# Kernel optimization log

Measured on AMD Instinct MI355X. Metric: run time of the kernel, lower is better.

## Reference

```python
import jax, jax.numpy as jnp
import numpy as np

N_NODES = 16384   # dim_size (number of aggregation groups)
DEG = 16          # neighbors per node
H = 128           # hidden_dim
E = N_NODES * DEG # total neighbor rows


def setup_inputs() -> dict:
    key = jax.random.key(0)
    k1, k2, k3 = jax.random.split(key, 3)
    x = jax.random.normal(k1, (E, H), dtype=jnp.float32)
    # sorted segment ids, DEG neighbors per node (ragged in general; uniform here)
    index = jnp.repeat(jnp.arange(N_NODES, dtype=jnp.int32), DEG)
    # torch LSTM params: gates stacked [i, f, g, o] -> [4H, H]
    W_ih = jax.random.normal(k2, (4 * H, H), dtype=jnp.float32) * 0.02  # xavier gain=0.02 scale
    W_hh = jax.random.normal(k3, (4 * H, H), dtype=jnp.float32) * (1.0 / np.sqrt(H))
    b_ih = jnp.zeros((4 * H,), jnp.float32)
    b_hh = jnp.zeros((4 * H,), jnp.float32)
    return {"x": x, "index": index, "W_ih": W_ih, "W_hh": W_hh,
            "b_ih": b_ih, "b_hh": b_hh, "dim_size": N_NODES}


def reference(x, index, W_ih, W_hh, b_ih, b_hh, dim_size):
    # Faithful to LSTMAggregator.forward: per-group gather of neighbor rows,
    # single-layer LSTM over each group's sequence, final hidden state h_n
    # written to out[group]; empty groups stay zero. (The original's randperm
    # shuffle is nondeterministic and omitted: neighbors kept in index order.)
    x = jnp.nan_to_num(x, nan=0.0)
    E_, Hd = x.shape

    # --- pack ragged groups into a padded [N, L, H] tensor ---
    order = jnp.argsort(index, stable=True)
    idx_s = index[order]
    counts = jax.ops.segment_sum(jnp.ones((E_,), jnp.int32), idx_s, num_segments=dim_size)
    starts = jnp.cumsum(counts) - counts           # exclusive prefix sum
    pos = jnp.arange(E_, dtype=jnp.int32) - starts[idx_s]  # position within group
    L = int(jnp.max(counts))                       # static at call time (concrete inputs)

    x_s = x[order]
    padded = jnp.zeros((dim_size, L, Hd), x.dtype).at[idx_s, pos].set(x_s)  # [N, L, H]
    valid = jnp.arange(L)[None, :] < counts[:, None]                        # [N, L]

    # --- batched masked LSTM scan over time ---
    bias = b_ih + b_hh
    h0 = jnp.zeros((dim_size, Hd), x.dtype)

    def step(carry, inp):
        h, c = carry
        xt, m = inp                                 # xt: [N, H], m: [N]
        gates = xt @ W_ih.T + h @ W_hh.T + bias     # [N, 4H], gate order i,f,g,o
        i, f, g, o = jnp.split(gates, 4, axis=-1)
        i = jax.nn.sigmoid(i); f = jax.nn.sigmoid(f)
        g = jnp.tanh(g);       o = jax.nn.sigmoid(o)
        c_new = f * c + i * g
        h_new = o * jnp.tanh(c_new)
        m = m[:, None]
        return (jnp.where(m, h_new, h), jnp.where(m, c_new, c)), None

    xs = (jnp.swapaxes(padded, 0, 1), valid.T)      # time-major [L, N, H], [L, N]
    (h_final, _), _ = jax.lax.scan(step, (h0, h0), xs)
    return jnp.nan_to_num(h_final, nan=0.0)        # [dim_size, H]
```

## Files before the change

### kernel.cpp

```cpp
#include <hip/hip_runtime.h>

#define DEG      16
#define HDIM     128
#define MB       32
#define NTHREADS 512

typedef __attribute__((ext_vector_type(8))) short  short8;
typedef __attribute__((ext_vector_type(4))) float  floatx4;
typedef __attribute__((ext_vector_type(4))) unsigned int uintx4;

#define MFMA(A,B,C) __builtin_amdgcn_mfma_f32_16x16x32_bf16(A,B,C,0,0,0)
#define L2E  1.4426950408889634f
#define L2E2 2.8853900817779268f

__device__ __forceinline__ unsigned short f2bf(float f) {
  union { float f; unsigned int u; } v; v.f = f;
  unsigned int u = v.u;
  u += 0x7fffu + ((u >> 16) & 1u);
  return (unsigned short)(u >> 16);
}

__device__ __forceinline__ unsigned int cvtpk(float lo, float hi) {
  unsigned int r;
  asm("v_cvt_pk_bf16_f32 %0, %1, %2" : "=v"(r) : "v"(lo), "v"(hi));
  return r;
}

#if __has_builtin(__builtin_amdgcn_exp2f)
#define FEXP2(x) __builtin_amdgcn_exp2f(x)
#else
__device__ __forceinline__ float FEXP2_fn(float x) {
  float r; asm("v_exp_f32 %0, %1" : "=v"(r) : "v"(x)); return r;
}
#define FEXP2(x) FEXP2_fn(x)
#endif

__device__ __forceinline__ float fsig2(float s) {
  return __builtin_amdgcn_rcpf(1.0f + FEXP2(-s));
}
__device__ __forceinline__ float ftanh2(float s) {
  return 1.0f - 2.0f * __builtin_amdgcn_rcpf(1.0f + FEXP2(s));
}

__global__ void convert_w_kernel(const float* __restrict__ Wih,
                                 const float* __restrict__ Whh,
                                 unsigned short* __restrict__ Wsw) {
  int i    = blockIdx.x * 256 + threadIdx.x;
  int lane = i & 63;
  int frag = i >> 6;
  int kt = frag >> 5;
  int wg = frag & 31;
  int w  = wg >> 2;
  int g  = wg & 3;
  int j  = g * 128 + w * 16 + (lane & 15);
  int k0 = kt * 32 + (lane >> 4) * 8;
  float sc = (g == 2) ? L2E2 : L2E;
  const float* src = (k0 < HDIM) ? (Wih + (size_t)j * HDIM + k0)
                                 : (Whh + (size_t)j * HDIM + (k0 - HDIM));
  short8 o;
  #pragma unroll
  for (int e = 0; e < 8; ++e) o[e] = (short)f2bf(src[e] * sc);
  *(short8*)(Wsw + (size_t)i * 8) = o;
}


#define HPART(HOFF)                                                            \
  {                                                                            \
    const unsigned short* Wp = Wsw;                                            \
    asm volatile("" : "+s"(Wp));                     \
    _Pragma("unroll")                                                          \
    for (int kh = 0; kh < 4; ++kh) {                                           \
      const unsigned short* Wk = Wp + ((size_t)((4 + kh) * 32 + w_id * 4) * 64 + lane) * 8; \
      short8 bfr[4];                                                           \
      _Pragma("unroll")                                                        \
      for (int g = 0; g < 4; ++g) bfr[g] = *(const short8*)(Wk + g * 512);     \
      const char* hb = (kh & 1) ? hsO : hsE;                                   \
      short8 ah0 = *(const short8*)(hb + (HOFF) + 0    + kh * 64);             \
      short8 ah1 = *(const short8*)(hb + (HOFF) + 4096 + kh * 64);             \
      _Pragma("unroll")                                                        \
      for (int g = 0; g < 4; ++g) {                                            \
        acc[g][0] = MFMA(ah0, bfr[g], acc[g][0]);                              \
        acc[g][1] = MFMA(ah1, bfr[g], acc[g][1]);                              \
      }                                                                        \
    }                                                                          \
  }

#define ACT1(MT, WOFF, LAST_, CS)                                              \
  {                                                                            \
    float hv[4];                                                               \
    _Pragma("unroll")                                                          \
    for (int r = 0; r < 4; ++r) {                                              \
      float iv = fsig2 (acc[0][MT][r]);                                        \
      float fv = fsig2 (acc[1][MT][r]);                                        \
      float gv = ftanh2(acc[2][MT][r]);                                        \
      float ov = fsig2 (acc[3][MT][r]);                                        \
      float cn = fv * CS[r] + iv * gv;                                         \
      CS[r] = cn;                                                              \
      hv[r] = ov * ftanh2(L2E2 * cn);                                          \
    }                                                                          \
    if (LAST_) {                                                               \
      float* ob = out + (size_t)(node0 + (MT) * 16 + q * 4) * HDIM + j_g;      \
      _Pragma("unroll")                                                        \
      for (int r = 0; r < 4; ++r) ob[r * HDIM] = hv[r];                        \
    } else {                                                                   \
      unsigned int p01 = cvtpk(hv[0], hv[1]);                                  \
      unsigned int p23 = cvtpk(hv[2], hv[3]);                                  \
      *(unsigned short*)(hwp[0] + (WOFF) + (MT) * 4096) = (unsigned short)p01;         \
      *(unsigned short*)(hwp[1] + (WOFF) + (MT) * 4096) = (unsigned short)(p01 >> 16); \
      *(unsigned short*)(hwp[2] + (WOFF) + (MT) * 4096) = (unsigned short)p23;         \
      *(unsigned short*)(hwp[3] + (WOFF) + (MT) * 4096) = (unsigned short)(p23 >> 16); \
    }                                                                          \
  }

#define XPART(XOFF)                                                            \
  {                                                                            \
    const unsigned short* Wp = Wsw;                                            \
    asm volatile("" : "+s"(Wp));                                               \
    const unsigned short* Wx = Wp + ((size_t)(w_id * 256 + lane)) * 8;         \
    short8 wv[4]; short8 a0, a1;                                               \
                                    \
    _Pragma("unroll")                                                          \
    for (int g = 0; g < 4; ++g) wv[g] = *(const short8*)(Wx + g * 512);        \
    a0 = *(const short8*)(xsE + (XOFF) + 0);                                   \
    a1 = *(const short8*)(xsE + (XOFF) + 4096 + 0);                            \
    _Pragma("unroll")                                                          \
    for (int g = 0; g < 4; ++g) {                                              \
      acc[g][0] = MFMA(a0, wv[g], bias4[g]);                                   \
      acc[g][1] = MFMA(a1, wv[g], bias4[g]);                                   \
    }                                                                          \
                                                                 \
    _Pragma("unroll")                                                          \
    for (int g = 0; g < 4; ++g) wv[g] = *(const short8*)(Wx + 16384 + g * 512);\
    a0 = *(const short8*)(xsO + (XOFF) + 64);                                  \
    a1 = *(const short8*)(xsO + (XOFF) + 4096 + 64);                           \
    _Pragma("unroll")                                                          \
    for (int g = 0; g < 4; ++g) {                                              \
      acc[g][0] = MFMA(a0, wv[g], acc[g][0]);                                  \
      acc[g][1] = MFMA(a1, wv[g], acc[g][1]);                                  \
    }                                                                          \
                                                                \
    _Pragma("unroll")                                                          \
    for (int g = 0; g < 4; ++g) wv[g] = *(const short8*)(wlB + g * 1024);      \
    a0 = *(const short8*)(xsE + (XOFF) + 128);                                 \
    a1 = *(const short8*)(xsE + (XOFF) + 4096 + 128);                          \
    _Pragma("unroll")                                                          \
    for (int g = 0; g < 4; ++g) {                                              \
      acc[g][0] = MFMA(a0, wv[g], acc[g][0]);                                  \
      acc[g][1] = MFMA(a1, wv[g], acc[g][1]);                                  \
    }                                                                          \
                                                                 \
    _Pragma("unroll")                                                          \
    for (int g = 0; g < 4; ++g) wv[g] = *(const short8*)(Wx + 49152 + g * 512);\
    a0 = *(const short8*)(xsO + (XOFF) + 192);                                 \
    a1 = *(const short8*)(xsO + (XOFF) + 4096 + 192);                          \
    _Pragma("unroll")                                                          \
    for (int g = 0; g < 4; ++g) {                                              \
      acc[g][0] = MFMA(a0, wv[g], acc[g][0]);                                  \
      acc[g][1] = MFMA(a1, wv[g], acc[g][1]);                                  \
    }                                                                          \
  }

#define STEP(T, PAR, WITH_H, LAST_)                                            \
  {                                                                            \
    if (WITH_H) HPART((PAR) * 8192);                                           \
    ACT1(0, ((PAR) ^ 1) * 8192, LAST_, cs0)                                    \
    ACT1(1, ((PAR) ^ 1) * 8192, LAST_, cs1)                                    \
    if (!(LAST_)) {                                                            \
      XPART((((PAR) ^ 1)) * 8192)                                              \
      if ((T) + 2 < DEG) {                                                     \
        uintx4 p;                                                              \
        p[0] = cvtpk(xp0[0], xp0[1]); p[1] = cvtpk(xp0[2], xp0[3]);            \
        p[2] = cvtpk(xp1[0], xp1[1]); p[3] = cvtpk(xp1[2], xp1[3]);            \
        *(uintx4*)(xsW + (PAR) * 8192) = p;                                    \
        if ((T) + 3 < DEG) {                                                   \
          const float* xq_ = xb0 + (size_t)((T) + 3) * HDIM;                   \
          xp0 = ((const floatx4*)xq_)[0]; xp1 = ((const floatx4*)xq_)[1];      \
        }                                                                      \
      }                                                                        \
    }                                                                          \
    __syncthreads();                                                           \
  }

__global__ __launch_bounds__(NTHREADS, 4)
void lstm_agg_kernel(const float* __restrict__ x,
                     const float* __restrict__ b_ih,
                     const float* __restrict__ b_hh,
                     const unsigned short* __restrict__ Wsw,
                     float* __restrict__ out) {
  __shared__ __align__(16) unsigned short Xs[2 * MB * HDIM];
  __shared__ __align__(16) unsigned short Hs[2 * MB * HDIM];
  __shared__ __align__(16) unsigned short Wl[32 * 512];

  const int tid  = threadIdx.x;
  const int w_id = tid >> 6;
  const int lane = tid & 63;
  const int l15  = lane & 15;
  const int q    = lane >> 4;
  const int node0 = blockIdx.x * MB;
  const int j_g = w_id * 16 + l15;

  floatx4 bias4[4];
  #pragma unroll
  for (int g = 0; g < 4; ++g) {
    float b = (b_ih[g * 128 + j_g] + b_hh[g * 128 + j_g]) * ((g == 2) ? L2E2 : L2E);
    floatx4 bv = {b, b, b, b};
    bias4[g] = bv;
  }

  #pragma unroll
  for (int i = 0; i < 4; ++i) {
    int o = tid * 32 + i * 8;
    *(short8*)&Wl[o] = *(const short8*)(Wsw + 2 * 32 * 512 + o);
  }

  const int fA  = (l15 & 7) ^ ((l15 & 8) >> 2);
  const int qx  = (q ^ (fA & 3)) << 4;
  const int f64 = (fA >> 2) << 6;
  const char* xsE = (const char*)Xs + l15 * 256 + qx + f64;
  const char* xsO = (const char*)Xs + l15 * 256 + qx - f64;
  const char* hsE = (const char*)Hs + l15 * 256 + qx + f64;
  const char* hsO = (const char*)Hs + l15 * 256 + qx - f64;

  const char* wlB = (const char*)Wl + w_id * 4096 + lane * 16;

  const int hc  = j_g >> 3;
  const int hkl = j_g & 7;
  char* hwp[4];
  #pragma unroll
  for (int r = 0; r < 4; ++r) {
    int m  = q * 4 + r;
    int fr = (m & 7) ^ ((m & 8) >> 2);
    hwp[r] = (char*)Hs + m * 256 + ((hc ^ fr) << 4) + hkl * 2;
  }

  const int m_x = tid >> 4;
  const int kc  = tid & 15;
  const int fX  = (m_x & 7) ^ ((m_x & 8) >> 2);
  const float* xb0 = x + ((size_t)(node0 + m_x) * DEG) * HDIM + kc * 8;
  char* xsW = (char*)Xs + m_x * 256 + ((kc ^ fX) << 4);

  floatx4 cs0 = {0.f, 0.f, 0.f, 0.f};
  floatx4 cs1 = {0.f, 0.f, 0.f, 0.f};
  floatx4 acc[4][2];
  floatx4 xp0, xp1;

  {
    floatx4 u0 = ((const floatx4*)xb0)[0], u1 = ((const floatx4*)xb0)[1];
    uintx4 p;
    p[0] = cvtpk(u0[0], u0[1]); p[1] = cvtpk(u0[2], u0[3]);
    p[2] = cvtpk(u1[0], u1[1]); p[3] = cvtpk(u1[2], u1[3]);
    *(uintx4*)xsW = p;
    u0 = ((const floatx4*)(xb0 + HDIM))[0]; u1 = ((const floatx4*)(xb0 + HDIM))[1];
    p[0] = cvtpk(u0[0], u0[1]); p[1] = cvtpk(u0[2], u0[3]);
    p[2] = cvtpk(u1[0], u1[1]); p[3] = cvtpk(u1[2], u1[3]);
    *(uintx4*)(xsW + 8192) = p;
    xp0 = ((const floatx4*)(xb0 + 2 * HDIM))[0];
    xp1 = ((const floatx4*)(xb0 + 2 * HDIM))[1];
  }
  __syncthreads();

  XPART(0)
  __syncthreads();

  STEP(0, 0, 0, 0)
  #pragma unroll 1
  for (int t = 1; t < 15; t += 2) {
    STEP(t,     1, 1, 0)
    STEP(t + 1, 0, 1, 0)
  }
  STEP(15, 1, 1, 1)
}

extern "C" void kernel_launch(void* const* d_in, const int* in_sizes, int n_in,
                              void* d_out, int out_size, void* d_ws, size_t ws_size,
                              hipStream_t stream) {
  const float* x   = (const float*)d_in[0];
  const float* Wih = (const float*)d_in[2];
  const float* Whh = (const float*)d_in[3];
  const float* bih = (const float*)d_in[4];
  const float* bhh = (const float*)d_in[5];
  unsigned short* Wsw = (unsigned short*)d_ws;
  float* out = (float*)d_out;

  hipLaunchKernelGGL(convert_w_kernel, dim3(64), dim3(256), 0, stream, Wih, Whh, Wsw);

  int nodes   = in_sizes[0] / (DEG * HDIM);
  int nblocks = nodes / MB;
  hipLaunchKernelGGL(lstm_agg_kernel, dim3(nblocks), dim3(NTHREADS), 0, stream,
                     x, bih, bhh, Wsw, out);
}
```

Baseline: 284.8 us.

## Process two 32-node tiles per block and interleave their gate activations with input MFMAs

Each block now handles 64 nodes as two 32-node sub-tiles. The recurrent MFMA pass covers both tiles, and one tile's activations are interleaved with the other tile's input-projection MFMAs so transcendental work overlaps matrix work. Three W_ih k-slices are held in registers, and a second W_hh slice moves into LDS using 128 KB of dynamic shared memory. The bias is added in the activation step instead of seeding the accumulator. In exchange, occupancy drops to 2 blocks per CU, register pressure rises, and the grid has half as many blocks.

Result: faster. 262.6 us (-7.8%).

```diff
diff --git a/kernel.cpp b/kernel.cpp
--- a/kernel.cpp
+++ b/kernel.cpp
@@ -2,7 +2,7 @@
 
 #define DEG      16
 #define HDIM     128
-#define MB       32
+#define MB       64
 #define NTHREADS 512
 
 typedef __attribute__((ext_vector_type(8))) short  short8;
@@ -26,14 +26,9 @@
   return r;
 }
 
-#if __has_builtin(__builtin_amdgcn_exp2f)
-#define FEXP2(x) __builtin_amdgcn_exp2f(x)
-#else
-__device__ __forceinline__ float FEXP2_fn(float x) {
+__device__ __forceinline__ float FEXP2(float x) {
   float r; asm("v_exp_f32 %0, %1" : "=v"(r) : "v"(x)); return r;
 }
-#define FEXP2(x) FEXP2_fn(x)
-#endif
 
 __device__ __forceinline__ float fsig2(float s) {
   return __builtin_amdgcn_rcpf(1.0f + FEXP2(-s));
@@ -64,132 +59,143 @@
 }
 
 
-#define HPART(HOFF)                                                            \
+#define HPART_BOTH(PAR)                                                        \
   {                                                                            \
     const unsigned short* Wp = Wsw;                                            \
     asm volatile("" : "+s"(Wp));                     \
     _Pragma("unroll")                                                          \
     for (int kh = 0; kh < 4; ++kh) {                                           \
-      const unsigned short* Wk = Wp + ((size_t)((4 + kh) * 32 + w_id * 4) * 64 + lane) * 8; \
       short8 bfr[4];                                                           \
-      _Pragma("unroll")                                                        \
-      for (int g = 0; g < 4; ++g) bfr[g] = *(const short8*)(Wk + g * 512);     \
+      if (kh == 2) {                                                           \
+        _Pragma("unroll")                                                      \
+        for (int g = 0; g < 4; ++g) bfr[g] = *(const short8*)(wlB6 + g * 1024);\
+      } else {                                                                 \
+        const unsigned short* Wk = Wp + ((size_t)((4 + kh) * 32 + w_id * 4) * 64 + lane) * 8; \
+        _Pragma("unroll")                                                      \
+        for (int g = 0; g < 4; ++g) bfr[g] = *(const short8*)(Wk + g * 512);   \
+      }                                                                        \
       const char* hb = (kh & 1) ? hsO : hsE;                                   \
-      short8 ah0 = *(const short8*)(hb + (HOFF) + 0    + kh * 64);             \
-      short8 ah1 = *(const short8*)(hb + (HOFF) + 4096 + kh * 64);             \
+      short8 a00 = *(const short8*)(hb + (PAR) * 16384 + 0     + kh * 64);     \
+      short8 a01 = *(const short8*)(hb + (PAR) * 16384 + 4096  + kh * 64);     \
+      short8 a10 = *(const short8*)(hb + (PAR) * 16384 + 8192  + kh * 64);     \
+      short8 a11 = *(const short8*)(hb + (PAR) * 16384 + 12288 + kh * 64);     \
       _Pragma("unroll")                                                        \
       for (int g = 0; g < 4; ++g) {                                            \
-        acc[g][0] = MFMA(ah0, bfr[g], acc[g][0]);                              \
-        acc[g][1] = MFMA(ah1, bfr[g], acc[g][1]);                              \
+        acc[0][g][0] = MFMA(a00, bfr[g], acc[0][g][0]);                        \
+        acc[0][g][1] = MFMA(a01, bfr[g], acc[0][g][1]);                        \
+        acc[1][g][0] = MFMA(a10, bfr[g], acc[1][g][0]);                        \
+        acc[1][g][1] = MFMA(a11, bfr[g], acc[1][g][1]);                        \
       }                                                                        \
     }                                                                          \
   }
 
-#define ACT1(MT, WOFF, LAST_, CS)                                              \
+#define ACT1(TAU, MT, WOFF, LAST_)                                             \
   {                                                                            \
     float hv[4];                                                               \
     _Pragma("unroll")                                                          \
     for (int r = 0; r < 4; ++r) {                                              \
-      float iv = fsig2 (acc[0][MT][r]);                                        \
-      float fv = fsig2 (acc[1][MT][r]);                                        \
-      float gv = ftanh2(acc[2][MT][r]);                                        \
-      float ov = fsig2 (acc[3][MT][r]);                                        \
-      float cn = fv * CS[r] + iv * gv;                                         \
-      CS[r] = cn;                                                              \
+      float iv = fsig2 (acc[TAU][0][MT][r] + bias[0]);                         \
+      float fv = fsig2 (acc[TAU][1][MT][r] + bias[1]);                         \
+      float gv = ftanh2(acc[TAU][2][MT][r] + bias[2]);                         \
+      float ov = fsig2 (acc[TAU][3][MT][r] + bias[3]);                         \
+      float cn = fv * cs[TAU][MT][r] + iv * gv;                                \
+      cs[TAU][MT][r] = cn;                                                     \
       hv[r] = ov * ftanh2(L2E2 * cn);                                          \
     }                                                                          \
     if (LAST_) {                                                               \
-      float* ob = out + (size_t)(node0 + (MT) * 16 + q * 4) * HDIM + j_g;      \
+      float* ob = outB + (TAU) * 4096 + (MT) * 2048;                           \
       _Pragma("unroll")                                                        \
       for (int r = 0; r < 4; ++r) ob[r * HDIM] = hv[r];                        \
     } else {                                                                   \
       unsigned int p01 = cvtpk(hv[0], hv[1]);                                  \
       unsigned int p23 = cvtpk(hv[2], hv[3]);                                  \
-      *(unsigned short*)(hwp[0] + (WOFF) + (MT) * 4096) = (unsigned short)p01;         \
-      *(unsigned short*)(hwp[1] + (WOFF) + (MT) * 4096) = (unsigned short)(p01 >> 16); \
-      *(unsigned short*)(hwp[2] + (WOFF) + (MT) * 4096) = (unsigned short)p23;         \
-      *(unsigned short*)(hwp[3] + (WOFF) + (MT) * 4096) = (unsigned short)(p23 >> 16); \
-    }                                                                          \
-  }
-
-#define XPART(XOFF)                                                            \
-  {                                                                            \
-    const unsigned short* Wp = Wsw;                                            \
-    asm volatile("" : "+s"(Wp));                                               \
-    const unsigned short* Wx = Wp + ((size_t)(w_id * 256 + lane)) * 8;         \
-    short8 wv[4]; short8 a0, a1;                                               \
-                                    \
-    _Pragma("unroll")                                                          \
-    for (int g = 0; g < 4; ++g) wv[g] = *(const short8*)(Wx + g * 512);        \
-    a0 = *(const short8*)(xsE + (XOFF) + 0);                                   \
-    a1 = *(const short8*)(xsE + (XOFF) + 4096 + 0);                            \
+      *(unsigned short*)(hwp[0] + (WOFF) + (TAU) * 8192 + (MT) * 4096) = (unsigned short)p01;         \
+      *(unsigned short*)(hwp[1] + (WOFF) + (TAU) * 8192 + (MT) * 4096) = (unsigned short)(p01 >> 16); \
+      *(unsigned short*)(hwp[2] + (WOFF) + (TAU) * 8192 + (MT) * 4096) = (unsigned short)p23;         \
+      *(unsigned short*)(hwp[3] + (WOFF) + (TAU) * 8192 + (MT) * 4096) = (unsigned short)(p23 >> 16); \
+    }                                                                          \
+  }
+
+#define XPART1(TAU, XOFF)                                                      \
+  {                                                                            \
+    floatx4 z4 = {0.0f, 0.0f, 0.0f, 0.0f};                                     \
+    short8 a0, a1, wv[4];                                                      \
+                                                   \
+    a0 = *(const short8*)(xsE + (XOFF) + (TAU) * 8192 + 0);                    \
+    a1 = *(const short8*)(xsE + (XOFF) + (TAU) * 8192 + 4096 + 0);             \
     _Pragma("unroll")                                                          \
     for (int g = 0; g < 4; ++g) {                                              \
-      acc[g][0] = MFMA(a0, wv[g], bias4[g]);                                   \
-      acc[g][1] = MFMA(a1, wv[g], bias4[g]);                                   \
-    }                                                                          \
-                                                                 \
-    _Pragma("unroll")                                                          \
-    for (int g = 0; g < 4; ++g) wv[g] = *(const short8*)(Wx + 16384 + g * 512);\
-    a0 = *(const short8*)(xsO + (XOFF) + 64);                                  \
-    a1 = *(const short8*)(xsO + (XOFF) + 4096 + 64);                           \
+      acc[TAU][g][0] = MFMA(a0, breg[0][g], z4);                               \
+      acc[TAU][g][1] = MFMA(a1, breg[0][g], z4);                               \
+    }                                                                          \
+                                                               \
+    a0 = *(const short8*)(xsO + (XOFF) + (TAU) * 8192 + 64);                   \
+    a1 = *(const short8*)(xsO + (XOFF) + (TAU) * 8192 + 4096 + 64);            \
     _Pragma("unroll")                                                          \
     for (int g = 0; g < 4; ++g) {                                              \
-      acc[g][0] = MFMA(a0, wv[g], acc[g][0]);                                  \
-      acc[g][1] = MFMA(a1, wv[g], acc[g][1]);                                  \
+      acc[TAU][g][0] = MFMA(a0, breg[1][g], acc[TAU][g][0]);                   \
+      acc[TAU][g][1] = MFMA(a1, breg[1][g], acc[TAU][g][1]);                   \
     }                                                                          \
                                                                 \
     _Pragma("unroll")                                                          \
     for (int g = 0; g < 4; ++g) wv[g] = *(const short8*)(wlB + g * 1024);      \
-    a0 = *(const short8*)(xsE + (XOFF) + 128);                                 \
-    a1 = *(const short8*)(xsE + (XOFF) + 4096 + 128);                          \
+    a0 = *(const short8*)(xsE + (XOFF) + (TAU) * 8192 + 128);                  \
+    a1 = *(const short8*)(xsE + (XOFF) + (TAU) * 8192 + 4096 + 128);           \
     _Pragma("unroll")                                                          \
     for (int g = 0; g < 4; ++g) {                                              \
-      acc[g][0] = MFMA(a0, wv[g], acc[g][0]);                                  \
-      acc[g][1] = MFMA(a1, wv[g], acc[g][1]);                                  \
-    }                                                                          \
-                                                                 \
-    _Pragma("unroll")                                                          \
-    for (int g = 0; g < 4; ++g) wv[g] = *(const short8*)(Wx + 49152 + g * 512);\
-    a0 = *(const short8*)(xsO + (XOFF) + 192);                                 \
-    a1 = *(const short8*)(xsO + (XOFF) + 4096 + 192);                          \
+      acc[TAU][g][0] = MFMA(a0, wv[g], acc[TAU][g][0]);                        \
+      acc[TAU][g][1] = MFMA(a1, wv[g], acc[TAU][g][1]);                        \
+    }                                                                          \
+                                                               \
+    a0 = *(const short8*)(xsO + (XOFF) + (TAU) * 8192 + 192);                  \
+    a1 = *(const short8*)(xsO + (XOFF) + (TAU) * 8192 + 4096 + 192);           \
     _Pragma("unroll")                                                          \
     for (int g = 0; g < 4; ++g) {                                              \
-      acc[g][0] = MFMA(a0, wv[g], acc[g][0]);                                  \
-      acc[g][1] = MFMA(a1, wv[g], acc[g][1]);                                  \
+      acc[TAU][g][0] = MFMA(a0, breg[2][g], acc[TAU][g][0]);                   \
+      acc[TAU][g][1] = MFMA(a1, breg[2][g], acc[TAU][g][1]);                   \
+    }                                                                          \
+  }
+
+#define STAGEX(TAU, PAR, T)                                                    \
+  {                                                                            \
+    uintx4 p;                                                                  \
+    p[0] = cvtpk(xp[TAU][0][0], xp[TAU][0][1]);                                \
+    p[1] = cvtpk(xp[TAU][0][2], xp[TAU][0][3]);                                \
+    p[2] = cvtpk(xp[TAU][1][0], xp[TAU][1][1]);                                \
+    p[3] = cvtpk(xp[TAU][1][2], xp[TAU][1][3]);                                \
+    *(uintx4*)(xsW + (PAR) * 16384 + (TAU) * 8192) = p;                        \
+    if ((T) + 3 < DEG) {                                                       \
+      const float* xq_ = xb[TAU] + (size_t)((T) + 3) * HDIM;                   \
+      xp[TAU][0] = ((const floatx4*)xq_)[0];                                   \
+      xp[TAU][1] = ((const floatx4*)xq_)[1];                                   \
     }                                                                          \
   }
 
 #define STEP(T, PAR, WITH_H, LAST_)                                            \
   {                                                                            \
-    if (WITH_H) HPART((PAR) * 8192);                                           \
-    ACT1(0, ((PAR) ^ 1) * 8192, LAST_, cs0)                                    \
-    ACT1(1, ((PAR) ^ 1) * 8192, LAST_, cs1)                                    \
+    if (WITH_H) HPART_BOTH(PAR);                                               \
+    ACT1(0, 0, ((PAR) ^ 1) * 16384, LAST_)                                     \
+    ACT1(0, 1, ((PAR) ^ 1) * 16384, LAST_)                                     \
+    if (!(LAST_)) XPART1(0, ((PAR) ^ 1) * 16384)                               \
+    ACT1(1, 0, ((PAR) ^ 1) * 16384, LAST_)                                     \
+    ACT1(1, 1, ((PAR) ^ 1) * 16384, LAST_)                                     \
     if (!(LAST_)) {                                                            \
-      XPART((((PAR) ^ 1)) * 8192)                                              \
+      XPART1(1, ((PAR) ^ 1) * 16384)                                           \
       if ((T) + 2 < DEG) {                                                     \
-        uintx4 p;                                                              \
-        p[0] = cvtpk(xp0[0], xp0[1]); p[1] = cvtpk(xp0[2], xp0[3]);            \
-        p[2] = cvtpk(xp1[0], xp1[1]); p[3] = cvtpk(xp1[2], xp1[3]);            \
-        *(uintx4*)(xsW + (PAR) * 8192) = p;                                    \
-        if ((T) + 3 < DEG) {                                                   \
-          const float* xq_ = xb0 + (size_t)((T) + 3) * HDIM;                   \
-          xp0 = ((const floatx4*)xq_)[0]; xp1 = ((const floatx4*)xq_)[1];      \
-        }                                                                      \
+        STAGEX(0, PAR, T)                                                      \
+        STAGEX(1, PAR, T)                                                      \
       }                                                                        \
     }                                                                          \
     __syncthreads();                                                           \
   }
 
-__global__ __launch_bounds__(NTHREADS, 4)
+__global__ __launch_bounds__(NTHREADS, 2)
 void lstm_agg_kernel(const float* __restrict__ x,
                      const float* __restrict__ b_ih,
                      const float* __restrict__ b_hh,
                      const unsigned short* __restrict__ Wsw,
                      float* __restrict__ out) {
-  __shared__ __align__(16) unsigned short Xs[2 * MB * HDIM];
-  __shared__ __align__(16) unsigned short Hs[2 * MB * HDIM];
-  __shared__ __align__(16) unsigned short Wl[32 * 512];
+  extern __shared__ char ldsb[];
 
   const int tid  = threadIdx.x;
   const int w_id = tid >> 6;
@@ -199,29 +205,39 @@
   const int node0 = blockIdx.x * MB;
   const int j_g = w_id * 16 + l15;
 
-  floatx4 bias4[4];
+  float bias[4];
+  #pragma unroll
+  for (int g = 0; g < 4; ++g)
+    bias[g] = (b_ih[g * 128 + j_g] + b_hh[g * 128 + j_g]) * ((g == 2) ? L2E2 : L2E);
+
+  short8 breg[3][4];
   #pragma unroll
   for (int g = 0; g < 4; ++g) {
-    float b = (b_ih[g * 128 + j_g] + b_hh[g * 128 + j_g]) * ((g == 2) ? L2E2 : L2E);
-    floatx4 bv = {b, b, b, b};
-    bias4[g] = bv;
-  }
-
-  #pragma unroll
-  for (int i = 0; i < 4; ++i) {
-    int o = tid * 32 + i * 8;
-    *(short8*)&Wl[o] = *(const short8*)(Wsw + 2 * 32 * 512 + o);
+    breg[0][g] = *(const short8*)(Wsw + ((size_t)(0 * 32 + w_id * 4 + g) * 64 + lane) * 8);
+    breg[1][g] = *(const short8*)(Wsw + ((size_t)(1 * 32 + w_id * 4 + g) * 64 + lane) * 8);
+    breg[2][g] = *(const short8*)(Wsw + ((size_t)(3 * 32 + w_id * 4 + g) * 64 + lane) * 8);
+  }
+
+  {
+    unsigned short* Wl = (unsigned short*)(ldsb + 65536);
+    #pragma unroll
+    for (int i = 0; i < 4; ++i) {
+      int o = tid * 32 + i * 8;
+      *(short8*)&Wl[o]          = *(const short8*)(Wsw + 2 * 16384 + o);
+      *(short8*)&Wl[16384 + o]  = *(const short8*)(Wsw + 6 * 16384 + o);
+    }
   }
 
   const int fA  = (l15 & 7) ^ ((l15 & 8) >> 2);
   const int qx  = (q ^ (fA & 3)) << 4;
   const int f64 = (fA >> 2) << 6;
-  const char* xsE = (const char*)Xs + l15 * 256 + qx + f64;
-  const char* xsO = (const char*)Xs + l15 * 256 + qx - f64;
-  const char* hsE = (const char*)Hs + l15 * 256 + qx + f64;
-  const char* hsO = (const char*)Hs + l15 * 256 + qx - f64;
-
-  const char* wlB = (const char*)Wl + w_id * 4096 + lane * 16;
+  const char* xsE = ldsb + l15 * 256 + qx + f64;
+  const char* xsO = ldsb + l15 * 256 + qx - f64;
+  const char* hsE = ldsb + 32768 + l15 * 256 + qx + f64;
+  const char* hsO = ldsb + 32768 + l15 * 256 + qx - f64;
+
+  const char* wlB  = ldsb + 65536 + w_id * 4096 + lane * 16;
+  const char* wlB6 = ldsb + 98304 + w_id * 4096 + lane * 16;
 
   const int hc  = j_g >> 3;
   const int hkl = j_g & 7;
@@ -230,36 +246,45 @@
   for (int r = 0; r < 4; ++r) {
     int m  = q * 4 + r;
     int fr = (m & 7) ^ ((m & 8) >> 2);
-    hwp[r] = (char*)Hs + m * 256 + ((hc ^ fr) << 4) + hkl * 2;
+    hwp[r] = ldsb + 32768 + m * 256 + ((hc ^ fr) << 4) + hkl * 2;
   }
 
   const int m_x = tid >> 4;
   const int kc  = tid & 15;
   const int fX  = (m_x & 7) ^ ((m_x & 8) >> 2);
-  const float* xb0 = x + ((size_t)(node0 + m_x) * DEG) * HDIM + kc * 8;
-  char* xsW = (char*)Xs + m_x * 256 + ((kc ^ fX) << 4);
-
-  floatx4 cs0 = {0.f, 0.f, 0.f, 0.f};
-  floatx4 cs1 = {0.f, 0.f, 0.f, 0.f};
-  floatx4 acc[4][2];
-  floatx4 xp0, xp1;
-
-  {
-    floatx4 u0 = ((const floatx4*)xb0)[0], u1 = ((const floatx4*)xb0)[1];
+  const float* xb[2];
+  xb[0] = x + ((size_t)(node0 + m_x) * DEG) * HDIM + kc * 8;
+  xb[1] = x + ((size_t)(node0 + 32 + m_x) * DEG) * HDIM + kc * 8;
+  char* xsW = ldsb + m_x * 256 + ((kc ^ fX) << 4);
+
+  float* outB = out + (size_t)(node0 + q * 4) * HDIM + j_g;
+
+  floatx4 cs[2][2];
+  #pragma unroll
+  for (int ta = 0; ta < 2; ++ta)
+    #pragma unroll
+    for (int mt = 0; mt < 2; ++mt) { floatx4 z = {0.f,0.f,0.f,0.f}; cs[ta][mt] = z; }
+  floatx4 acc[2][4][2];
+  floatx4 xp[2][2];
+
+  #pragma unroll
+  for (int ta = 0; ta < 2; ++ta) {
+    floatx4 u0 = ((const floatx4*)xb[ta])[0], u1 = ((const floatx4*)xb[ta])[1];
     uintx4 p;
     p[0] = cvtpk(u0[0], u0[1]); p[1] = cvtpk(u0[2], u0[3]);
     p[2] = cvtpk(u1[0], u1[1]); p[3] = cvtpk(u1[2], u1[3]);
-    *(uintx4*)xsW = p;
-    u0 = ((const floatx4*)(xb0 + HDIM))[0]; u1 = ((const floatx4*)(xb0 + HDIM))[1];
+    *(uintx4*)(xsW + ta * 8192) = p;
+    u0 = ((const floatx4*)(xb[ta] + HDIM))[0]; u1 = ((const floatx4*)(xb[ta] + HDIM))[1];
     p[0] = cvtpk(u0[0], u0[1]); p[1] = cvtpk(u0[2], u0[3]);
     p[2] = cvtpk(u1[0], u1[1]); p[3] = cvtpk(u1[2], u1[3]);
-    *(uintx4*)(xsW + 8192) = p;
-    xp0 = ((const floatx4*)(xb0 + 2 * HDIM))[0];
-    xp1 = ((const floatx4*)(xb0 + 2 * HDIM))[1];
+    *(uintx4*)(xsW + 16384 + ta * 8192) = p;
+    xp[ta][0] = ((const floatx4*)(xb[ta] + 2 * HDIM))[0];
+    xp[ta][1] = ((const floatx4*)(xb[ta] + 2 * HDIM))[1];
   }
   __syncthreads();
 
-  XPART(0)
+  XPART1(0, 0)
+  XPART1(1, 0)
   __syncthreads();
 
   STEP(0, 0, 0, 0)
@@ -282,10 +307,18 @@
   unsigned short* Wsw = (unsigned short*)d_ws;
   float* out = (float*)d_out;
 
+  static bool attr_done = false;
+  if (!attr_done) {
+    (void)hipFuncSetAttribute((const void*)lstm_agg_kernel,
+                              hipFuncAttributeMaxDynamicSharedMemorySize,
+                              131072);
+    attr_done = true;
+  }
+
   hipLaunchKernelGGL(convert_w_kernel, dim3(64), dim3(256), 0, stream, Wih, Whh, Wsw);
 
   int nodes   = in_sizes[0] / (DEG * HDIM);
   int nblocks = nodes / MB;
-  hipLaunchKernelGGL(lstm_agg_kernel, dim3(nblocks), dim3(NTHREADS), 0, stream,
+  hipLaunchKernelGGL(lstm_agg_kernel, dim3(nblocks), dim3(NTHREADS), 131072, stream,
                      x, bih, bhh, Wsw, out);
 }
```
